# Performance work log

Hardware: AMD Instinct MI355X
Metric: run time of the kernel (lower is better)

The kernel has to match this reference:

```python
import jax, jax.numpy as jnp
import numpy as np


def setup_inputs() -> dict:
    key = jax.random.key(0)
    ks = jax.random.split(key, 5)
    B, S, D, F = 4, 2048, 1024, 4096
    scale_w1 = 1.0 / np.sqrt(D)
    scale_w2 = 1.0 / np.sqrt(F)
    return {
        "hidden_states": jax.random.normal(ks[0], (B, S, D), dtype=jnp.float32),
        "W1": jax.random.normal(ks[1], (F, D), dtype=jnp.float32) * scale_w1,
        "b1": jax.random.normal(ks[2], (F,), dtype=jnp.float32) * 0.02,
        "W2": jax.random.normal(ks[3], (D, F), dtype=jnp.float32) * scale_w2,
        "b2": jax.random.normal(ks[4], (D,), dtype=jnp.float32) * 0.02,
    }


def _sigmoid_poly(h):
    # cubic polynomial sigmoid approximation: 0.5 + 0.25*h - 0.0208*h^3
    h2 = h * h
    h3 = h2 * h
    return 0.5 + 0.25 * h + (-0.0208) * h3


def reference(hidden_states, W1, b1, W2, b2):
    # secure linear projection == plain affine: x @ W.T + b
    h = jnp.einsum("bsd,fd->bsf", hidden_states, W1) + b1  # [B,S,F]
    sw = h * _sigmoid_poly(h)                               # swish via poly sigmoid
    out = jnp.einsum("bsf,df->bsd", sw, W2) + b2            # [B,S,D]
    return out
```

## Files before the change

kernel.cpp:

```cpp
#include <hip/hip_runtime.h>
#include <hip/hip_bf16.h>

typedef __bf16 bf16_t;
typedef __bf16 bf16x8 __attribute__((ext_vector_type(8)));
typedef float f32x4 __attribute__((ext_vector_type(4)));

typedef const __attribute__((address_space(3))) bf16_t* lds_cptr;

__global__ __launch_bounds__(256) void cast3_f32_to_bf16(
    const float* __restrict__ a, bf16_t* __restrict__ ao, int na8,
    const float* __restrict__ b, bf16_t* __restrict__ bo, int nb8,
    const float* __restrict__ c, bf16_t* __restrict__ co, int nc8) {
  int i = blockIdx.x * blockDim.x + threadIdx.x;
  const float* in;
  bf16_t* out;
  int j;
  if (i < na8) {
    in = a; out = ao; j = i;
  } else if (i < na8 + nb8) {
    in = b; out = bo; j = i - na8;
  } else if (i < na8 + nb8 + nc8) {
    in = c; out = co; j = i - na8 - nb8;
  } else {
    return;
  }
  const float4* in4 = (const float4*)in;
  float4 f0 = in4[2 * j];
  float4 f1 = in4[2 * j + 1];
  bf16x8 o;
  o[0] = (bf16_t)f0.x; o[1] = (bf16_t)f0.y;
  o[2] = (bf16_t)f0.z; o[3] = (bf16_t)f0.w;
  o[4] = (bf16_t)f1.x; o[5] = (bf16_t)f1.y;
  o[6] = (bf16_t)f1.z; o[7] = (bf16_t)f1.w;
  ((bf16x8*)out)[j] = o;
}

__device__ __forceinline__ void gload_lds16(const bf16_t* g, bf16_t* l) {
  __builtin_amdgcn_global_load_lds(
      (const __attribute__((address_space(1))) void*)g,
      (__attribute__((address_space(3))) void*)l,
      16, 0, 0);
}

template <int N>
__device__ __forceinline__ void vmwait() {
  if constexpr (N == 3) asm volatile("s_waitcnt vmcnt(3)");
  else if constexpr (N == 4) asm volatile("s_waitcnt vmcnt(4)");
  else if constexpr (N == 6) asm volatile("s_waitcnt vmcnt(6)");
  else if constexpr (N == 8) asm volatile("s_waitcnt vmcnt(8)");
  else asm volatile("s_waitcnt vmcnt(0)");
}

template <int N>
__device__ __forceinline__ void lgkmwait() {
  asm volatile("s_waitcnt lgkmcnt(%0)" :: "i"(N));
}

template <int I, int N, int BOFF>
__device__ __forceinline__ void ldsr_n(bf16x8* dst, lds_cptr p) {
  if constexpr (I < N) {
    asm volatile("ds_read_b128 %0, %1 offset:%2"
                 : "=v"(dst[I]) : "v"(p), "i"(BOFF + I * 1024));
    ldsr_n<I + 1, N, BOFF>(dst, p);
  }
}

template <int I, int FR, int FC>
__device__ __forceinline__ void mfma_rows(const bf16x8* aq, const bf16x8* bq,
                                          f32x4 (&acc)[FR][FC]) {
  if constexpr (I < FR) {
    lgkmwait<FR - 1 - I>();
    __builtin_amdgcn_sched_barrier(0);
#pragma unroll
    for (int j = 0; j < FC; ++j)
      acc[I][j] = __builtin_amdgcn_mfma_f32_16x16x32_bf16(
          aq[I], bq[j], acc[I][j], 0, 0, 0);
    mfma_rows<I + 1, FR, FC>(aq, bq, acc);
  }
}

#define SMALL_TILE(s_, b_)                                                    \
  {                                                                           \
    int sw__ = (s_) + 3;                                                      \
    if (sw__ >= NS) sw__ -= NS;                                               \
    lds_cptr pa3 = sA3 + (b_) * (256 * 32) + aoff;                            \
    lds_cptr pb3 = sB3 + (b_) * (BN * 32) + boff;                             \
    bf16x8 bq[FC], aq[FR];                                                    \
    ldsr_n<0, FC, 0>(bq, pb3);                                                \
    ldsr_n<0, FR, 0>(aq, pa3);                                                \
    stageA(sw__);                                                             \
    stageB(sw__);                                                             \
    __builtin_amdgcn_s_setprio(1);                                            \
    mfma_rows<0, FR, FC>(aq, bq, acc);                                        \
    __builtin_amdgcn_s_setprio(0);                                            \
    vmwait<2 * VMN>();                                                        \
    __builtin_amdgcn_s_barrier();                                             \
  }

template <int BN, int WM, int WN, bool SWISH>
__global__ __launch_bounds__(512, 2) void gemm_bt8(
    const bf16_t* __restrict__ A, const bf16_t* __restrict__ B,
    const float* __restrict__ bias, void* __restrict__ Cout,
    int M, int N, int K, int XW, int px, int py) {
  constexpr int BM = 256;
  constexpr int WR = BM / WM;
  constexpr int WC = BN / WN;
  constexpr int FR = WR / 16;
  constexpr int FC = WC / 16;
  constexpr int ACALLS = BM / 128;
  constexpr int BCALLS = BN / 128;
  constexpr int VMN = ACALLS + BCALLS;

  const int tid = threadIdx.x;
  const int wave = tid >> 6;
  const int lane = tid & 63;

  const int bid = blockIdx.x;
  const int xcd = bid & 7;
  const int idx = bid >> 3;
  const int cx = xcd % XW;
  const int cy = xcd / XW;
  const int bx = cx * px + idx % px;
  const int by = cy * py + idx / px;
  const int tileM = by * BM;
  const int tileN = bx * BN;

  __shared__ __align__(16) bf16_t sA[4 * 256 * 32];
  __shared__ __align__(16) bf16_t sB[4 * BN * 32];
  lds_cptr sA3 = (lds_cptr)sA;
  lds_cptr sB3 = (lds_cptr)sB;

  const int srow = (wave << 4) + (lane >> 2);
  const int sgc = ((lane & 3) ^ ((lane >> 3) & 3)) << 3;
  const bf16_t* gA = A + (size_t)(tileM + srow) * K + sgc;
  const bf16_t* gB = B + (size_t)(tileN + srow) * K + sgc;
  bf16_t* lA = sA + (wave << 9);
  bf16_t* lB = sB + (wave << 9);

  auto stageA = [&](int s) {
    bf16_t* l = lA + (s & 3) * (256 * 32);
    const bf16_t* g = gA + s * 32;
#pragma unroll
    for (int c = 0; c < ACALLS; ++c)
      gload_lds16(g + (size_t)(c * 128) * K, l + c * 128 * 32);
  };
  auto stageB = [&](int s) {
    bf16_t* l = lB + (s & 3) * (BN * 32);
    const bf16_t* g = gB + s * 32;
#pragma unroll
    for (int c = 0; c < BCALLS; ++c)
      gload_lds16(g + (size_t)(c * 128) * K, l + c * 128 * 32);
  };

  const int wr = wave / WN;
  const int wc = wave % WN;
  const int fr = lane & 15;
  const int pc = (lane >> 4) ^ ((fr >> 1) & 3);
  const int aoff = (wr * WR + fr) * 32 + pc * 8;
  const int boff = (wc * WC + fr) * 32 + pc * 8;

  f32x4 acc[FR][FC] = {};

  const int NS = K >> 5;

  stageA(0); stageB(0);
  stageA(1); stageB(1);
  stageA(2); stageB(2);
  vmwait<2 * VMN>();
  __builtin_amdgcn_s_barrier();

  for (int os = 0; os < NS; os += 4) {
    SMALL_TILE(os + 0, 0)
    SMALL_TILE(os + 1, 1)
    SMALL_TILE(os + 2, 2)
    SMALL_TILE(os + 3, 3)
  }

  const int cRow0 = tileM + wr * WR + ((lane >> 4) << 2);
  const int cCol0 = tileN + wc * WC + (lane & 15);
  float bv[FC];
#pragma unroll
  for (int j = 0; j < FC; ++j) bv[j] = bias[cCol0 + j * 16];
#pragma unroll
  for (int i = 0; i < FR; ++i) {
#pragma unroll
    for (int r = 0; r < 4; ++r) {
      const size_t row = (size_t)(cRow0 + i * 16 + r);
#pragma unroll
      for (int j = 0; j < FC; ++j) {
        float h = acc[i][j][r] + bv[j];
        if constexpr (SWISH) {
          float h3 = h * h * h;
          float sw = h * (0.5f + 0.25f * h - 0.0208f * h3);
          ((bf16_t*)Cout)[row * N + cCol0 + j * 16] = (bf16_t)sw;
        } else {
          ((float*)Cout)[row * N + cCol0 + j * 16] = h;
        }
      }
    }
  }
}

extern "C" void kernel_launch(void* const* d_in, const int* in_sizes, int n_in,
                              void* d_out, int out_size, void* d_ws,
                              size_t ws_size, hipStream_t stream) {
  const float* X  = (const float*)d_in[0];
  const float* W1 = (const float*)d_in[1];
  const float* b1 = (const float*)d_in[2];
  const float* W2 = (const float*)d_in[3];
  const float* b2 = (const float*)d_in[4];
  float* out = (float*)d_out;

  const int F = in_sizes[2];
  const int D = in_sizes[4];
  const int M = in_sizes[0] / D;

  bf16_t* Xb  = (bf16_t*)d_ws;
  bf16_t* W1b = Xb + (size_t)M * D;
  bf16_t* W2b = W1b + (size_t)F * D;
  bf16_t* SW  = W2b + (size_t)D * F;

  const int nX = (M * D) / 8, nW1 = (F * D) / 8, nW2 = (D * F) / 8;
  const int nTot = nX + nW1 + nW2;
  cast3_f32_to_bf16<<<(nTot + 255) / 256, 256, 0, stream>>>(
      X, Xb, nX, W1, W1b, nW1, W2, W2b, nW2);

  {
    const int gx = F / 256, gy = M / 256;
    const int XW = 2, XH = 4;
    const int px = gx / XW, py = gy / XH;
    gemm_bt8<256, 2, 4, true><<<gx * gy, 512, 0, stream>>>(
        Xb, W1b, b1, (void*)SW, M, F, D, XW, px, py);
  }

  {
    const int gx = D / 128, gy = M / 256;
    const int XW = 1, XH = 8;
    const int px = gx / XW, py = gy / XH;
    gemm_bt8<128, 4, 2, false><<<gx * gy, 512, 0, stream>>>(
        SW, W2b, b2, (void*)out, M, D, F, XW, px, py);
  }
}
```

Before: 241.2 us.

## Switch GEMMs to BK=64 triple-buffered 256x128 tiles with split LDS reads

Both GEMMs now use one kernel with a 256x128 output tile and a K-step of 64 instead of 32. It keeps three LDS stages with rotating read/write offsets and a new 8-way XOR swizzle. Each iteration issues two half-K sets of ds_reads, and the second set overlaps the MFMAs of the first via lgkmcnt gating. The first GEMM drops from a 256x256 tile to 256x128, and the XCD grid mapping changes for both launches. The aim is to halve barriers and waits per K, at the cost of a smaller first-GEMM tile (less reuse) and different LDS and register pressure.

```diff
diff --git a/kernel.cpp b/kernel.cpp
--- a/kernel.cpp
+++ b/kernel.cpp
@@ -44,11 +44,7 @@
 
 template <int N>
 __device__ __forceinline__ void vmwait() {
-  if constexpr (N == 3) asm volatile("s_waitcnt vmcnt(3)");
-  else if constexpr (N == 4) asm volatile("s_waitcnt vmcnt(4)");
-  else if constexpr (N == 6) asm volatile("s_waitcnt vmcnt(6)");
-  else if constexpr (N == 8) asm volatile("s_waitcnt vmcnt(8)");
-  else asm volatile("s_waitcnt vmcnt(0)");
+  asm volatile("s_waitcnt vmcnt(%0)" :: "i"(N));
 }
 
 template <int N>
@@ -56,60 +52,62 @@
   asm volatile("s_waitcnt lgkmcnt(%0)" :: "i"(N));
 }
 
-template <int I, int N, int BOFF>
+template <int I, int N, int STRIDE_B>
 __device__ __forceinline__ void ldsr_n(bf16x8* dst, lds_cptr p) {
   if constexpr (I < N) {
     asm volatile("ds_read_b128 %0, %1 offset:%2"
-                 : "=v"(dst[I]) : "v"(p), "i"(BOFF + I * 1024));
-    ldsr_n<I + 1, N, BOFF>(dst, p);
-  }
-}
-
-template <int I, int FR, int FC>
-__device__ __forceinline__ void mfma_rows(const bf16x8* aq, const bf16x8* bq,
-                                          f32x4 (&acc)[FR][FC]) {
+                 : "=v"(dst[I]) : "v"(p), "i"(I * STRIDE_B));
+    ldsr_n<I + 1, N, STRIDE_B>(dst, p);
+  }
+}
+
+template <int I, int FR, int FC, int BASE>
+__device__ __forceinline__ void mfma_gated(const bf16x8* aq, const bf16x8* bq,
+                                           f32x4 (&acc)[FR][FC]) {
   if constexpr (I < FR) {
-    lgkmwait<FR - 1 - I>();
+    lgkmwait<BASE - I>();
     __builtin_amdgcn_sched_barrier(0);
 #pragma unroll
     for (int j = 0; j < FC; ++j)
       acc[I][j] = __builtin_amdgcn_mfma_f32_16x16x32_bf16(
           aq[I], bq[j], acc[I][j], 0, 0, 0);
-    mfma_rows<I + 1, FR, FC>(aq, bq, acc);
-  }
-}
-
-#define SMALL_TILE(s_, b_)                                                    \
+    mfma_gated<I + 1, FR, FC, BASE>(aq, bq, acc);
+  }
+}
+
+#define BODY(rA_, rB_, wA_, wB_, sw_)                                         \
   {                                                                           \
-    int sw__ = (s_) + 3;                                                      \
-    if (sw__ >= NS) sw__ -= NS;                                               \
-    lds_cptr pa3 = sA3 + (b_) * (256 * 32) + aoff;                            \
-    lds_cptr pb3 = sB3 + (b_) * (BN * 32) + boff;                             \
-    bf16x8 bq[FC], aq[FR];                                                    \
-    ldsr_n<0, FC, 0>(bq, pb3);                                                \
-    ldsr_n<0, FR, 0>(aq, pa3);                                                \
-    stageA(sw__);                                                             \
-    stageB(sw__);                                                             \
+    lds_cptr pa0 = (lds_cptr)(sA + (rA_)) + aoff0;                            \
+    lds_cptr pb0 = (lds_cptr)(sB + (rB_)) + boff0;                            \
+    lds_cptr pa1 = (lds_cptr)(sA + (rA_)) + aoff1;                            \
+    lds_cptr pb1 = (lds_cptr)(sB + (rB_)) + boff1;                            \
+    bf16x8 b0[FC], a0[FR], b1[FC], a1[FR];                                    \
+    ldsr_n<0, FC, 2048>(b0, pb0);                                             \
+    ldsr_n<0, FR, 2048>(a0, pa0);                                             \
+    stageA(sw_, wA_);                                                         \
+    stageB(sw_, wB_);                                                         \
+    ldsr_n<0, FC, 2048>(b1, pb1);                                             \
+    ldsr_n<0, FR, 2048>(a1, pa1);                                             \
     __builtin_amdgcn_s_setprio(1);                                            \
-    mfma_rows<0, FR, FC>(aq, bq, acc);                                        \
+    mfma_gated<0, FR, FC, FR + FC + FR - 1>(a0, b0, acc);                     \
+    mfma_gated<0, FR, FC, FR - 1>(a1, b1, acc);                               \
     __builtin_amdgcn_s_setprio(0);                                            \
-    vmwait<2 * VMN>();                                                        \
+    vmwait<VMN>();                                                            \
     __builtin_amdgcn_s_barrier();                                             \
   }
 
-template <int BN, int WM, int WN, bool SWISH>
-__global__ __launch_bounds__(512, 2) void gemm_bt8(
+template <bool SWISH>
+__global__ __launch_bounds__(512, 2) void gemm_bt64(
     const bf16_t* __restrict__ A, const bf16_t* __restrict__ B,
     const float* __restrict__ bias, void* __restrict__ Cout,
     int M, int N, int K, int XW, int px, int py) {
-  constexpr int BM = 256;
-  constexpr int WR = BM / WM;
-  constexpr int WC = BN / WN;
-  constexpr int FR = WR / 16;
-  constexpr int FC = WC / 16;
-  constexpr int ACALLS = BM / 128;
-  constexpr int BCALLS = BN / 128;
+  constexpr int BM = 256, BN = 128, BK = 64;
+  constexpr int FR = 4, FC = 4;
+  constexpr int ACALLS = BM / 64;
+  constexpr int BCALLS = BN / 64;
   constexpr int VMN = ACALLS + BCALLS;
+  constexpr int SA_SZ = BM * BK;
+  constexpr int SB_SZ = BN * BK;
 
   const int tid = threadIdx.x;
   const int wave = tid >> 6;
@@ -125,59 +123,61 @@
   const int tileM = by * BM;
   const int tileN = bx * BN;
 
-  __shared__ __align__(16) bf16_t sA[4 * 256 * 32];
-  __shared__ __align__(16) bf16_t sB[4 * BN * 32];
-  lds_cptr sA3 = (lds_cptr)sA;
-  lds_cptr sB3 = (lds_cptr)sB;
-
-  const int srow = (wave << 4) + (lane >> 2);
-  const int sgc = ((lane & 3) ^ ((lane >> 3) & 3)) << 3;
+  __shared__ __align__(16) bf16_t sA[3 * SA_SZ];
+  __shared__ __align__(16) bf16_t sB[3 * SB_SZ];
+
+  const int srow = (wave << 3) + (lane >> 3);
+  const int sgc = ((lane & 7) ^ ((lane >> 3) & 7)) << 3;
   const bf16_t* gA = A + (size_t)(tileM + srow) * K + sgc;
   const bf16_t* gB = B + (size_t)(tileN + srow) * K + sgc;
-  bf16_t* lA = sA + (wave << 9);
-  bf16_t* lB = sB + (wave << 9);
-
-  auto stageA = [&](int s) {
-    bf16_t* l = lA + (s & 3) * (256 * 32);
-    const bf16_t* g = gA + s * 32;
+
+  auto stageA = [&](int s, int wb) {
+    bf16_t* l = sA + wb + (wave << 9);
+    const bf16_t* g = gA + s * BK;
 #pragma unroll
     for (int c = 0; c < ACALLS; ++c)
-      gload_lds16(g + (size_t)(c * 128) * K, l + c * 128 * 32);
+      gload_lds16(g + (size_t)(c * 64) * K, l + c * 4096);
   };
-  auto stageB = [&](int s) {
-    bf16_t* l = lB + (s & 3) * (BN * 32);
-    const bf16_t* g = gB + s * 32;
+  auto stageB = [&](int s, int wb) {
+    bf16_t* l = sB + wb + (wave << 9);
+    const bf16_t* g = gB + s * BK;
 #pragma unroll
     for (int c = 0; c < BCALLS; ++c)
-      gload_lds16(g + (size_t)(c * 128) * K, l + c * 128 * 32);
+      gload_lds16(g + (size_t)(c * 64) * K, l + c * 4096);
   };
 
-  const int wr = wave / WN;
-  const int wc = wave % WN;
+  const int wr = wave >> 1;
+  const int wc = wave & 1;
   const int fr = lane & 15;
-  const int pc = (lane >> 4) ^ ((fr >> 1) & 3);
-  const int aoff = (wr * WR + fr) * 32 + pc * 8;
-  const int boff = (wc * WC + fr) * 32 + pc * 8;
+  const int pc0 = (lane >> 4) ^ (fr & 7);
+  const int aoff0 = (wr * 64 + fr) * 64 + pc0 * 8;
+  const int boff0 = (wc * 64 + fr) * 64 + pc0 * 8;
+  const int aoff1 = aoff0 ^ 32;
+  const int boff1 = boff0 ^ 32;
 
   f32x4 acc[FR][FC] = {};
 
-  const int NS = K >> 5;
-
-  stageA(0); stageB(0);
-  stageA(1); stageB(1);
-  stageA(2); stageB(2);
-  vmwait<2 * VMN>();
+  const int NSB = K >> 6;
+
+  stageA(0, 0);          stageB(0, 0);
+  stageA(1, SA_SZ);      stageB(1, SB_SZ);
+  vmwait<VMN>();
   __builtin_amdgcn_s_barrier();
 
-  for (int os = 0; os < NS; os += 4) {
-    SMALL_TILE(os + 0, 0)
-    SMALL_TILE(os + 1, 1)
-    SMALL_TILE(os + 2, 2)
-    SMALL_TILE(os + 3, 3)
-  }
-
-  const int cRow0 = tileM + wr * WR + ((lane >> 4) << 2);
-  const int cCol0 = tileN + wc * WC + (lane & 15);
+  int rA = 0, rB = 0;
+  int wA = 2 * SA_SZ, wB = 2 * SB_SZ;
+  for (int s = 0; s < NSB; ++s) {
+    int sw = s + 2;
+    if (sw >= NSB) sw -= NSB;
+    BODY(rA, rB, wA, wB, sw)
+    rA = (rA == 2 * SA_SZ) ? 0 : rA + SA_SZ;
+    rB = (rB == 2 * SB_SZ) ? 0 : rB + SB_SZ;
+    wA = (wA == 2 * SA_SZ) ? 0 : wA + SA_SZ;
+    wB = (wB == 2 * SB_SZ) ? 0 : wB + SB_SZ;
+  }
+
+  const int cRow0 = tileM + wr * 64 + ((lane >> 4) << 2);
+  const int cCol0 = tileN + wc * 64 + (lane & 15);
   float bv[FC];
 #pragma unroll
   for (int j = 0; j < FC; ++j) bv[j] = bias[cCol0 + j * 16];
@@ -226,18 +226,18 @@
       X, Xb, nX, W1, W1b, nW1, W2, W2b, nW2);
 
   {
-    const int gx = F / 256, gy = M / 256;
+    const int gx = F / 128, gy = M / 256;
+    const int XW = 4, XH = 2;
+    const int px = gx / XW, py = gy / XH;
+    gemm_bt64<true><<<gx * gy, 512, 0, stream>>>(
+        Xb, W1b, b1, (void*)SW, M, F, D, XW, px, py);
+  }
+
+  {
+    const int gx = D / 128, gy = M / 256;
     const int XW = 2, XH = 4;
     const int px = gx / XW, py = gy / XH;
-    gemm_bt8<256, 2, 4, true><<<gx * gy, 512, 0, stream>>>(
-        Xb, W1b, b1, (void*)SW, M, F, D, XW, px, py);
-  }
-
-  {
-    const int gx = D / 128, gy = M / 256;
-    const int XW = 1, XH = 8;
-    const int px = gx / XW, py = gy / XH;
-    gemm_bt8<128, 4, 2, false><<<gx * gy, 512, 0, stream>>>(
+    gemm_bt64<false><<<gx * gy, 512, 0, stream>>>(
         SW, W2b, b2, (void*)out, M, D, F, XW, px, py);
   }
 }
```

Result: slower. 252.6 us (+4.8%).

## Double-buffer LDS fragment registers to overlap next-tile reads with MFMAs

Applied to the files above, without the earlier changes.

Restructures the GEMM main loop so the LDS-to-register fragment reads for the next K-step are issued midway through the current step's MFMA sequence, using two ping-pong register sets. This aims to hide ds_read latency behind matrix work instead of stalling at the start of each step. It roughly doubles the fragment register footprint, which risks spills or lower occupancy under the 512x2 launch bounds. The hand-tuned lgkmcnt counts must also match the interleaved read order exactly.

```diff
diff --git a/kernel.cpp b/kernel.cpp
--- a/kernel.cpp
+++ b/kernel.cpp
@@ -44,11 +44,7 @@
 
 template <int N>
 __device__ __forceinline__ void vmwait() {
-  if constexpr (N == 3) asm volatile("s_waitcnt vmcnt(3)");
-  else if constexpr (N == 4) asm volatile("s_waitcnt vmcnt(4)");
-  else if constexpr (N == 6) asm volatile("s_waitcnt vmcnt(6)");
-  else if constexpr (N == 8) asm volatile("s_waitcnt vmcnt(8)");
-  else asm volatile("s_waitcnt vmcnt(0)");
+  asm volatile("s_waitcnt vmcnt(%0)" :: "i"(N));
 }
 
 template <int N>
@@ -56,44 +52,48 @@
   asm volatile("s_waitcnt lgkmcnt(%0)" :: "i"(N));
 }
 
-template <int I, int N, int BOFF>
-__device__ __forceinline__ void ldsr_n(bf16x8* dst, lds_cptr p) {
-  if constexpr (I < N) {
+template <int I, int E>
+__device__ __forceinline__ void ldsr_rng(bf16x8* dst, lds_cptr p) {
+  if constexpr (I < E) {
     asm volatile("ds_read_b128 %0, %1 offset:%2"
-                 : "=v"(dst[I]) : "v"(p), "i"(BOFF + I * 1024));
-    ldsr_n<I + 1, N, BOFF>(dst, p);
-  }
-}
-
-template <int I, int FR, int FC>
-__device__ __forceinline__ void mfma_rows(const bf16x8* aq, const bf16x8* bq,
-                                          f32x4 (&acc)[FR][FC]) {
-  if constexpr (I < FR) {
-    lgkmwait<FR - 1 - I>();
+                 : "=v"(dst[I]) : "v"(p), "i"(I * 1024));
+    ldsr_rng<I + 1, E>(dst, p);
+  }
+}
+
+template <int I, int END, int FR, int FC, int BASE>
+__device__ __forceinline__ void mfma_gr(const bf16x8 (&aq)[FR],
+                                        const bf16x8 (&bq)[FC],
+                                        f32x4 (&acc)[FR][FC]) {
+  if constexpr (I < END) {
+    lgkmwait<BASE - I>();
     __builtin_amdgcn_sched_barrier(0);
 #pragma unroll
     for (int j = 0; j < FC; ++j)
       acc[I][j] = __builtin_amdgcn_mfma_f32_16x16x32_bf16(
           aq[I], bq[j], acc[I][j], 0, 0, 0);
-    mfma_rows<I + 1, FR, FC>(aq, bq, acc);
-  }
-}
-
-#define SMALL_TILE(s_, b_)                                                    \
+    mfma_gr<I + 1, END, FR, FC, BASE>(aq, bq, acc);
+  }
+}
+
+#define BODY(bc_, bn_, sw_, AC, BC, AN, BNX)                                  \
   {                                                                           \
-    int sw__ = (s_) + 3;                                                      \
-    if (sw__ >= NS) sw__ -= NS;                                               \
-    lds_cptr pa3 = sA3 + (b_) * (256 * 32) + aoff;                            \
-    lds_cptr pb3 = sB3 + (b_) * (BN * 32) + boff;                             \
-    bf16x8 bq[FC], aq[FR];                                                    \
-    ldsr_n<0, FC, 0>(bq, pb3);                                                \
-    ldsr_n<0, FR, 0>(aq, pa3);                                                \
-    stageA(sw__);                                                             \
-    stageB(sw__);                                                             \
+    stageA(sw_);                                                              \
+    stageB(sw_);                                                              \
+    __builtin_amdgcn_sched_barrier(0);                                        \
     __builtin_amdgcn_s_setprio(1);                                            \
-    mfma_rows<0, FR, FC>(aq, bq, acc);                                        \
+    mfma_gr<0, FR / 2, FR, FC, FR - 1>(AC, BC, acc);                          \
     __builtin_amdgcn_s_setprio(0);                                            \
     vmwait<2 * VMN>();                                                        \
+    __builtin_amdgcn_sched_barrier(0);                                        \
+    lds_cptr paN = sA3 + (bn_) * (256 * 32) + aoff;                           \
+    lds_cptr pbN = sB3 + (bn_) * (BN * 32) + boff;                            \
+    ldsr_rng<0, FC>(BNX, pbN);                                                \
+    ldsr_rng<0, 2>(AN, paN);                                                  \
+    __builtin_amdgcn_s_setprio(1);                                            \
+    mfma_gr<FR / 2, FR, FR, FC, FR + 5>(AC, BC, acc);                         \
+    __builtin_amdgcn_s_setprio(0);                                            \
+    ldsr_rng<2, FR>(AN, paN);                                                 \
     __builtin_amdgcn_s_barrier();                                             \
   }
 
@@ -160,6 +160,7 @@
   const int boff = (wc * WC + fr) * 32 + pc * 8;
 
   f32x4 acc[FR][FC] = {};
+  bf16x8 aR0[FR], bR0[FC], aR1[FR], bR1[FC];
 
   const int NS = K >> 5;
 
@@ -168,13 +169,22 @@
   stageA(2); stageB(2);
   vmwait<2 * VMN>();
   __builtin_amdgcn_s_barrier();
+  __builtin_amdgcn_sched_barrier(0);
+  ldsr_rng<0, FC>(bR0, sB3 + boff);
+  ldsr_rng<0, FR>(aR0, sA3 + aoff);
 
   for (int os = 0; os < NS; os += 4) {
-    SMALL_TILE(os + 0, 0)
-    SMALL_TILE(os + 1, 1)
-    SMALL_TILE(os + 2, 2)
-    SMALL_TILE(os + 3, 3)
-  }
+    int w0 = os + 3;     if (w0 >= NS) w0 -= NS;
+    int w1 = os + 4;     if (w1 >= NS) w1 -= NS;
+    int w2 = os + 5;     if (w2 >= NS) w2 -= NS;
+    int w3 = os + 6;     if (w3 >= NS) w3 -= NS;
+    BODY(0, 1, w0, aR0, bR0, aR1, bR1)
+    BODY(1, 2, w1, aR1, bR1, aR0, bR0)
+    BODY(2, 3, w2, aR0, bR0, aR1, bR1)
+    BODY(3, 0, w3, aR1, bR1, aR0, bR0)
+  }
+  lgkmwait<0>();
+  __builtin_amdgcn_sched_barrier(0);
 
   const int cRow0 = tileM + wr * WR + ((lane >> 4) << 2);
   const int cCol0 = tileN + wc * WC + (lane & 15);
```

New measurement: 245.8 us. About the same (+1.9%).
